# Performance work log

Hardware: AMD Instinct MI355X
Metric: run time of the kernel (lower is better)

Reference implementation:

```python
import jax, jax.numpy as jnp
import numpy as np

DIM, HEADS, WIN = 256, 8, 8
HD = DIM // HEADS
SCALE = HD ** -0.5


def _rel_index(w):
    # Swin-style relative position index, computed statically in numpy
    coords = np.stack(np.meshgrid(np.arange(w), np.arange(w), indexing='ij'))  # (2,w,w)
    cf = coords.reshape(2, -1)                      # (2, w*w)
    rel = (cf[:, :, None] - cf[:, None, :]).transpose(1, 2, 0)  # (w*w, w*w, 2)
    rel = rel.copy()
    rel[:, :, 0] += w - 1
    rel[:, :, 1] += w - 1
    rel[:, :, 0] *= 2 * w - 1
    return rel.sum(-1)                              # (w*w, w*w)

REL_IDX = _rel_index(WIN)


def setup_inputs() -> dict:
    key = jax.random.key(0)
    ks = jax.random.split(key, 6)
    B, C, D, H, W = 8, DIM, 100, WIN, WIN
    return {
        'x': jax.random.normal(ks[0], (B, C, D, H, W), jnp.float32),
        'dwconv_w': jax.random.normal(ks[1], (C, C, 1, 3, 3), jnp.float32) * 0.02,
        'dwconv_b': jnp.zeros((C,), jnp.float32),
        'qkv_w': jax.random.normal(ks[2], (3 * C, C), jnp.float32) * 0.02,
        'qkv_b': jnp.zeros((3 * C,), jnp.float32),
        'proj_w': jax.random.normal(ks[3], (C, C), jnp.float32) * 0.02,
        'proj_b': jnp.zeros((C,), jnp.float32),
        'rpb_table': jax.random.normal(ks[4], ((2 * WIN - 1) ** 2, HEADS), jnp.float32) * 0.02,
    }


def reference(x, dwconv_w, dwconv_b, qkv_w, qkv_b, proj_w, proj_b, rpb_table):
    B, C, D, H, W = x.shape
    N = H * W
    # 'dwconv': full Conv3d, kernel (1,3,3), padding (0,1,1)
    xl = jax.lax.conv_general_dilated(
        x, dwconv_w, window_strides=(1, 1, 1),
        padding=[(0, 0), (1, 1), (1, 1)],
        dimension_numbers=('NCDHW', 'OIDHW', 'NCDHW'),
    ) + dwconv_b[None, :, None, None, None]
    # qkv: 1x1x1 conv == pointwise linear over channels
    qkv = jnp.einsum('oc,bcdhw->bodhw', qkv_w, xl) + qkv_b[None, :, None, None, None]
    # channel dim layout: (three, head, head_dim)
    qkv = qkv.reshape(B, 3, HEADS, HD, D, N)
    q, k, v = qkv[:, 0], qkv[:, 1], qkv[:, 2]      # each (B, HEADS, HD, D, N)
    attn = jnp.einsum('bhcdn,bhcdm->bdhnm', q * SCALE, k)  # (B, D, HEADS, N, N)
    bias = rpb_table[REL_IDX.reshape(-1)].reshape(N, N, HEADS).transpose(2, 0, 1)
    attn = jax.nn.softmax(attn + bias[None, None], axis=-1)
    xa = jnp.einsum('bdhnm,bhcdm->bhcdn', attn, v)  # (B, HEADS, HD, D, N)
    xa = xa.reshape(B, C, D, H, W)                  # channel = (head, head_dim)
    out = jnp.einsum('oc,bcdhw->bodhw', proj_w, xa) + proj_b[None, :, None, None, None]
    return out
```

## Files before the change

kernel.cpp:

```cpp
#include <hip/hip_runtime.h>
#include <cstdint>
#include <cstddef>

#define SCALEQ 0.17677669529663689f

typedef _Float16 half_t;
typedef _Float16 half8   __attribute__((ext_vector_type(8)));
typedef _Float16 half4v  __attribute__((ext_vector_type(4)));
typedef float    float4v __attribute__((ext_vector_type(4)));

#define GLDS16(gp, lp)                                                        \
  __builtin_amdgcn_global_load_lds(                                           \
      (const __attribute__((address_space(1))) void*)(gp),                    \
      (__attribute__((address_space(3))) void*)(lp), 16, 0, 0)

__global__ __launch_bounds__(256) void prep_all(
    const float* __restrict__ x, const float* __restrict__ dwconv_w,
    const float* __restrict__ qkv_w, const float* __restrict__ proj_w,
    const float* __restrict__ rpb, half_t* __restrict__ xpad,
    half_t* __restrict__ Wt, half_t* __restrict__ qw16,
    half_t* __restrict__ pw16, float* __restrict__ btab) {
  __shared__ float tile[128 * 65];
  const int blk = blockIdx.x, t = threadIdx.x;
  if (blk < 800) {
    const int bd = blk, b = bd / 100, d = bd % 100;
    for (int hf = 0; hf < 2; ++hf) {
      for (int i = 0; i < 32; ++i) {
        int idx = i * 256 + t, c = idx >> 6, hw = idx & 63;
        tile[c * 65 + hw] = x[(size_t)((b * 256 + hf * 128 + c) * 100 + d) * 64 + hw];
      }
      __syncthreads();
      for (int i = 0; i < 50; ++i) {
        int idx = i * 256 + t, cell = idx >> 7, c = idx & 127;
        int hh = cell / 10, ww = cell % 10;
        float v = 0.f;
        if (hh >= 1 && hh <= 8 && ww >= 1 && ww <= 8)
          v = tile[c * 65 + (hh - 1) * 8 + (ww - 1)];
        xpad[(size_t)(bd * 100 + cell) * 256 + hf * 128 + c] = (half_t)v;
      }
      __syncthreads();
    }
  } else if (blk < 944) {
    const int base = (blk - 800) * 4096;
#pragma unroll
    for (int i = 0; i < 16; ++i) {
      int idx = base + i * 256 + t;
      int tap = idx >> 16;
      int og = (idx >> 12) & 15, kh = (idx >> 9) & 7;
      int l15o = (idx >> 5) & 15, c5 = idx & 31;
      int o = og * 16 + l15o, c = kh * 32 + c5;
      Wt[idx] = (half_t)dwconv_w[(o * 256 + c) * 9 + tap];
    }
  } else if (blk < 1040) {
    const int base = (blk - 944) * 2048;
#pragma unroll
    for (int i = 0; i < 8; ++i) {
      int idx = base + i * 256 + t;
      float v = qkv_w[idx];
      if (idx < 65536) v *= SCALEQ;
      qw16[idx] = (half_t)v;
    }
  } else if (blk < 1072) {
    const int base = (blk - 1040) * 2048;
#pragma unroll
    for (int i = 0; i < 8; ++i) {
      int idx = base + i * 256 + t;
      pw16[idx] = (half_t)proj_w[idx];
    }
  } else {
    const int base = (blk - 1072) * 2048;
#pragma unroll
    for (int i = 0; i < 8; ++i) {
      int idx = base + i * 256 + t;
      int hd = idx >> 12, n = (idx >> 6) & 63, m = idx & 63;
      int h1 = n >> 3, w1 = n & 7, h2 = m >> 3, w2 = m & 7;
      int ridx = (h1 - h2 + 7) * 15 + (w1 - w2 + 7);
      btab[idx] = rpb[ridx * 8 + hd];
    }
  }
}

__global__ __launch_bounds__(512) void fused_all(
    const half_t* __restrict__ xpg, const half_t* __restrict__ Wt,
    const float* __restrict__ convb, const half_t* __restrict__ qw,
    const float* __restrict__ qkvb, const float* __restrict__ btab,
    const half_t* __restrict__ pw, const float* __restrict__ projb,
    float* __restrict__ out32) {
  __shared__ __align__(16) half_t LS[78336];
  const int bd = blockIdx.x;
  const int tid = threadIdx.x;
  const int wave = tid >> 6, lane = tid & 63;
  const int l15 = lane & 15, quad = lane >> 4;
  const int head = wave;

  half_t* xlp = LS;
  half_t* xa = LS;
  float* T = (float*)LS;
  half_t* xpl = LS + 16896;
  half_t* scr = LS + 16896 + wave * 7680;
  half_t* qsc = scr;
  half_t* ksc = scr + 2560;
  half_t* vsc = scr + 5120;
  half_t* Psc = scr;

  const half_t* Wq0 = qw + head * 32 * 256;
  const half_t* Wk0 = qw + 65536 + head * 32 * 256;
  const half_t* Wv0 = qw + 131072 + head * 32 * 256;

  {
    const char* src = (const char*)(xpg + (size_t)bd * 25600);
    const int cid = wave * 64 + lane;
#pragma unroll
    for (int i = 0; i < 7; ++i) {
      const int chunkid = i * 512 + cid;
      if (chunkid < 3200) {
        const int cell = chunkid >> 5, p = chunkid & 31;
        const int g = (p & 24) | ((p ^ cell) & 7);
        GLDS16(src + cell * 512 + g * 16,
               (char*)xpl + (i * 512 + wave * 64) * 16);
      }
    }
  }
  __syncthreads();

  {
    const int pxb = (l15 >> 3) * 10 + (l15 & 7);
    float4v acc[2][4];
#pragma unroll
    for (int mi = 0; mi < 2; ++mi)
#pragma unroll
      for (int ni = 0; ni < 4; ++ni) {
        float4v z = {0.f, 0.f, 0.f, 0.f};
        acc[mi][ni] = z;
      }
    const half_t* wv0 = Wt + (wave * 2) * 4096 + l15 * 32 + quad * 8;
#pragma unroll 1
    for (int tap = 0; tap < 9; ++tap) {
      const int tc = (tap / 3) * 10 + (tap % 3);
      const half_t* wt = wv0 + tap * 65536;
      const int c0 = pxb + tc;
#pragma unroll
      for (int kh = 0; kh < 8; ++kh) {
        half8 af0 = *(const half8*)(wt + kh * 512);
        half8 af1 = *(const half8*)(wt + 4096 + kh * 512);
        half8 bf[4];
#pragma unroll
        for (int ni = 0; ni < 4; ++ni) {
          const int cell = c0 + ni * 20;
          bf[ni] = *(const half8*)&xpl[cell * 256 + (((kh * 4 + quad) ^ (cell & 7)) * 8)];
        }
#pragma unroll
        for (int ni = 0; ni < 4; ++ni) {
          acc[0][ni] = __builtin_amdgcn_mfma_f32_16x16x32_f16(af0, bf[ni], acc[0][ni], 0, 0, 0);
          acc[1][ni] = __builtin_amdgcn_mfma_f32_16x16x32_f16(af1, bf[ni], acc[1][ni], 0, 0, 0);
        }
      }
    }
#pragma unroll
    for (int mi = 0; mi < 2; ++mi) {
      const int o4 = wave * 32 + mi * 16 + quad * 4;
      const float4v b4 = *(const float4v*)&convb[o4];
      const int chunk = o4 >> 3;
      const int sub = (quad & 1) * 4;
#pragma unroll
      for (int ni = 0; ni < 4; ++ni) {
        const int px = ni * 16 + l15;
        half4v h;
        h.x = (half_t)(acc[mi][ni].x + b4.x);
        h.y = (half_t)(acc[mi][ni].y + b4.y);
        h.z = (half_t)(acc[mi][ni].z + b4.z);
        h.w = (half_t)(acc[mi][ni].w + b4.w);
        *(half4v*)&xlp[px * 256 + ((chunk ^ (px & 7)) * 8) + sub] = h;
      }
    }
  }

  half8 wq[8][2];
#pragma unroll
  for (int kh = 0; kh < 8; ++kh)
#pragma unroll
    for (int mi = 0; mi < 2; ++mi)
      wq[kh][mi] = *(const half8*)(Wq0 + (mi * 16 + l15) * 256 + kh * 32 + quad * 8);

  __syncthreads();

  half8 wk[8][2];
  {
    float4v acc[2][4];
#pragma unroll
    for (int mi = 0; mi < 2; ++mi)
#pragma unroll
      for (int ni = 0; ni < 4; ++ni) {
        float4v z = {0.f, 0.f, 0.f, 0.f};
        acc[mi][ni] = z;
      }
#pragma unroll
    for (int kh = 0; kh < 8; ++kh) {
      half8 bf[4];
#pragma unroll
      for (int ni = 0; ni < 4; ++ni) {
        int r = ni * 16 + l15;
        bf[ni] = *(const half8*)&xlp[r * 256 + (((kh * 4 + quad) ^ (r & 7)) * 8)];
      }
#pragma unroll
      for (int mi = 0; mi < 2; ++mi)
        wk[kh][mi] = *(const half8*)(Wk0 + (mi * 16 + l15) * 256 + kh * 32 + quad * 8);
#pragma unroll
      for (int mi = 0; mi < 2; ++mi)
#pragma unroll
        for (int ni = 0; ni < 4; ++ni)
          acc[mi][ni] = __builtin_amdgcn_mfma_f32_16x16x32_f16(
              wq[kh][mi], bf[ni], acc[mi][ni], 0, 0, 0);
    }
#pragma unroll
    for (int mi = 0; mi < 2; ++mi) {
      const float4v b4 = *(const float4v*)&qkvb[head * 32 + mi * 16 + quad * 4];
#pragma unroll
      for (int ni = 0; ni < 4; ++ni) {
        half4v h;
        h.x = (half_t)(acc[mi][ni].x + b4.x * SCALEQ);
        h.y = (half_t)(acc[mi][ni].y + b4.y * SCALEQ);
        h.z = (half_t)(acc[mi][ni].z + b4.z * SCALEQ);
        h.w = (half_t)(acc[mi][ni].w + b4.w * SCALEQ);
        *(half4v*)(qsc + (ni * 16 + l15) * 40 + mi * 16 + quad * 4) = h;
      }
    }
  }

  half8 wv[8][2];
  {
    float4v acc[2][4];
#pragma unroll
    for (int mi = 0; mi < 2; ++mi)
#pragma unroll
      for (int ni = 0; ni < 4; ++ni) {
        float4v z = {0.f, 0.f, 0.f, 0.f};
        acc[mi][ni] = z;
      }
#pragma unroll
    for (int kh = 0; kh < 8; ++kh) {
      half8 bf[4];
#pragma unroll
      for (int ni = 0; ni < 4; ++ni) {
        int r = ni * 16 + l15;
        bf[ni] = *(const half8*)&xlp[r * 256 + (((kh * 4 + quad) ^ (r & 7)) * 8)];
      }
#pragma unroll
      for (int mi = 0; mi < 2; ++mi)
        wv[kh][mi] = *(const half8*)(Wv0 + (mi * 16 + l15) * 256 + kh * 32 + quad * 8);
#pragma unroll
      for (int mi = 0; mi < 2; ++mi)
#pragma unroll
        for (int ni = 0; ni < 4; ++ni)
          acc[mi][ni] = __builtin_amdgcn_mfma_f32_16x16x32_f16(
              wk[kh][mi], bf[ni], acc[mi][ni], 0, 0, 0);
    }
#pragma unroll
    for (int mi = 0; mi < 2; ++mi) {
      const float4v b4 = *(const float4v*)&qkvb[256 + head * 32 + mi * 16 + quad * 4];
#pragma unroll
      for (int ni = 0; ni < 4; ++ni) {
        half4v h;
        h.x = (half_t)(acc[mi][ni].x + b4.x);
        h.y = (half_t)(acc[mi][ni].y + b4.y);
        h.z = (half_t)(acc[mi][ni].z + b4.z);
        h.w = (half_t)(acc[mi][ni].w + b4.w);
        *(half4v*)(ksc + (ni * 16 + l15) * 40 + mi * 16 + quad * 4) = h;
      }
    }
  }

  {
    float4v acc[2][4];
#pragma unroll
    for (int mi = 0; mi < 2; ++mi)
#pragma unroll
      for (int ni = 0; ni < 4; ++ni) {
        float4v z = {0.f, 0.f, 0.f, 0.f};
        acc[mi][ni] = z;
      }
#pragma unroll
    for (int kh = 0; kh < 8; ++kh) {
      half8 bf[4];
#pragma unroll
      for (int ni = 0; ni < 4; ++ni) {
        int r = ni * 16 + l15;
        bf[ni] = *(const half8*)&xlp[r * 256 + (((kh * 4 + quad) ^ (r & 7)) * 8)];
      }
#pragma unroll
      for (int mi = 0; mi < 2; ++mi)
#pragma unroll
        for (int ni = 0; ni < 4; ++ni)
          acc[mi][ni] = __builtin_amdgcn_mfma_f32_16x16x32_f16(
              wv[kh][mi], bf[ni], acc[mi][ni], 0, 0, 0);
    }
#pragma unroll
    for (int mi = 0; mi < 2; ++mi) {
      const float4v b4 = *(const float4v*)&qkvb[512 + head * 32 + mi * 16 + quad * 4];
#pragma unroll
      for (int ni = 0; ni < 4; ++ni) {
#pragma unroll
        for (int iv = 0; iv < 4; ++iv)
          vsc[(mi * 16 + quad * 4 + iv) * 72 + ni * 16 + l15] =
              (half_t)(acc[mi][ni][iv] + b4[iv]);
      }
    }
  }

  __builtin_amdgcn_s_waitcnt(0);

  half8 aq[4], bk[4];
#pragma unroll
  for (int i = 0; i < 4; ++i) {
    aq[i] = *(const half8*)(qsc + (i * 16 + l15) * 40 + quad * 8);
    bk[i] = *(const half8*)(ksc + (i * 16 + l15) * 40 + quad * 8);
  }
  const float* bh = btab + head * 4096;
  float br[4][4][4];
#pragma unroll
  for (int ni = 0; ni < 4; ++ni)
#pragma unroll
    for (int i = 0; i < 4; ++i) {
      const int n = ni * 16 + quad * 4 + i;
#pragma unroll
      for (int mi = 0; mi < 4; ++mi)
        br[ni][i][mi] = bh[n * 64 + mi * 16 + l15];
    }
  float4v s[4][4];
#pragma unroll
  for (int ni = 0; ni < 4; ++ni)
#pragma unroll
    for (int mi = 0; mi < 4; ++mi) {
      float4v z = {0.f, 0.f, 0.f, 0.f};
      s[ni][mi] = __builtin_amdgcn_mfma_f32_16x16x32_f16(aq[ni], bk[mi], z, 0, 0, 0);
    }
#pragma unroll
  for (int ni = 0; ni < 4; ++ni)
#pragma unroll
    for (int i = 0; i < 4; ++i)
#pragma unroll
      for (int mi = 0; mi < 4; ++mi) s[ni][mi][i] += br[ni][i][mi];
  float inv[4][4];
#pragma unroll
  for (int ni = 0; ni < 4; ++ni)
#pragma unroll
    for (int i = 0; i < 4; ++i) {
      float mx = fmaxf(fmaxf(s[ni][0][i], s[ni][1][i]), fmaxf(s[ni][2][i], s[ni][3][i]));
      for (int off = 1; off < 16; off <<= 1) mx = fmaxf(mx, __shfl_xor(mx, off));
      float sum = 0.f;
#pragma unroll
      for (int mi = 0; mi < 4; ++mi) {
        float e = __expf(s[ni][mi][i] - mx);
        s[ni][mi][i] = e;
        sum += e;
      }
      for (int off = 1; off < 16; off <<= 1) sum += __shfl_xor(sum, off);
      inv[ni][i] = 1.0f / sum;
    }
#pragma unroll
  for (int ni = 0; ni < 4; ++ni)
#pragma unroll
    for (int i = 0; i < 4; ++i) {
      const int n = ni * 16 + quad * 4 + i;
#pragma unroll
      for (int mi = 0; mi < 4; ++mi)
        Psc[n * 72 + mi * 16 + l15] = (half_t)(s[ni][mi][i] * inv[ni][i]);
    }
  __builtin_amdgcn_s_waitcnt(0);

  half8 wp[8][2];
#pragma unroll
  for (int kh = 0; kh < 8; ++kh)
#pragma unroll
    for (int mi = 0; mi < 2; ++mi)
      wp[kh][mi] = *(const half8*)(pw + (wave * 32 + mi * 16 + l15) * 256 + kh * 32 + quad * 8);
  half8 av[2][2];
#pragma unroll
  for (int ci = 0; ci < 2; ++ci)
#pragma unroll
    for (int k2 = 0; k2 < 2; ++k2)
      av[ci][k2] = *(const half8*)(vsc + (ci * 16 + l15) * 72 + k2 * 32 + quad * 8);
  float4v oa[2][4];
#pragma unroll
  for (int ci = 0; ci < 2; ++ci)
#pragma unroll
    for (int ni = 0; ni < 4; ++ni) {
      float4v z = {0.f, 0.f, 0.f, 0.f};
      oa[ci][ni] = z;
    }
#pragma unroll
  for (int ni = 0; ni < 4; ++ni)
#pragma unroll
    for (int k2 = 0; k2 < 2; ++k2) {
      half8 bp = *(const half8*)&Psc[(ni * 16 + l15) * 72 + k2 * 32 + quad * 8];
#pragma unroll
      for (int ci = 0; ci < 2; ++ci)
        oa[ci][ni] = __builtin_amdgcn_mfma_f32_16x16x32_f16(av[ci][k2], bp, oa[ci][ni], 0, 0, 0);
    }

  __syncthreads();

#pragma unroll
  for (int ci = 0; ci < 2; ++ci)
#pragma unroll
    for (int ni = 0; ni < 4; ++ni) {
      half4v h = {(half_t)oa[ci][ni].x, (half_t)oa[ci][ni].y,
                  (half_t)oa[ci][ni].z, (half_t)oa[ci][ni].w};
      *(half4v*)(xa + (ni * 16 + l15) * 264 + head * 32 + ci * 16 + quad * 4) = h;
    }
  __syncthreads();

  float4v pacc[2][4];
#pragma unroll
  for (int mi = 0; mi < 2; ++mi)
#pragma unroll
    for (int ni = 0; ni < 4; ++ni) {
      float4v z = {0.f, 0.f, 0.f, 0.f};
      pacc[mi][ni] = z;
    }
#pragma unroll
  for (int kh = 0; kh < 8; ++kh) {
    half8 bf[4];
#pragma unroll
    for (int ni = 0; ni < 4; ++ni)
      bf[ni] = *(const half8*)&xa[(ni * 16 + l15) * 264 + kh * 32 + quad * 8];
#pragma unroll
    for (int mi = 0; mi < 2; ++mi)
#pragma unroll
      for (int ni = 0; ni < 4; ++ni)
        pacc[mi][ni] = __builtin_amdgcn_mfma_f32_16x16x32_f16(
            wp[kh][mi], bf[ni], pacc[mi][ni], 0, 0, 0);
  }
#pragma unroll
  for (int mi = 0; mi < 2; ++mi) {
    const float4v b4 = *(const float4v*)&projb[wave * 32 + mi * 16 + quad * 4];
#pragma unroll
    for (int ni = 0; ni < 4; ++ni) {
      pacc[mi][ni].x += b4.x;
      pacc[mi][ni].y += b4.y;
      pacc[mi][ni].z += b4.z;
      pacc[mi][ni].w += b4.w;
    }
  }

  const int b = bd / 100, d = bd % 100;
  const size_t bdbase = (size_t)b * 1638400 + (size_t)d * 64;
  const int tr = tid >> 3;
  const int col0 = (tid & 7) * 8;
  for (int r = 0; r < 4; ++r) {
    __syncthreads();
    if ((wave >> 1) == r) {
      const int rb = (wave & 1) * 32;
#pragma unroll
      for (int mi = 0; mi < 2; ++mi)
#pragma unroll
        for (int ni = 0; ni < 4; ++ni)
#pragma unroll
          for (int iv = 0; iv < 4; ++iv)
            T[(rb + mi * 16 + quad * 4 + iv) * 68 + ni * 16 + l15] = pacc[mi][ni][iv];
    }
    __syncthreads();
    const int o = r * 64 + tr;
    float* dst = out32 + bdbase + (size_t)o * 6400 + col0;
    const float* srcT = &T[tr * 68 + col0];
    *(float4v*)dst = *(const float4v*)srcT;
    *(float4v*)(dst + 4) = *(const float4v*)(srcT + 4);
  }
}

extern "C" void kernel_launch(void* const* d_in, const int* in_sizes, int n_in,
                              void* d_out, int out_size, void* d_ws, size_t ws_size,
                              hipStream_t stream) {
  const float* x        = (const float*)d_in[0];
  const float* dwconv_w = (const float*)d_in[1];
  const float* dwconv_b = (const float*)d_in[2];
  const float* qkv_w    = (const float*)d_in[3];
  const float* qkv_b    = (const float*)d_in[4];
  const float* proj_w   = (const float*)d_in[5];
  const float* proj_b   = (const float*)d_in[6];
  const float* rpb      = (const float*)d_in[7];
  float* out = (float*)d_out;

  char* ws = (char*)d_ws;
  size_t off = 0;
  half_t* xpad = (half_t*)(ws + off); off += 40960000;
  half_t* Wt   = (half_t*)(ws + off); off += 1179648;
  half_t* qw16 = (half_t*)(ws + off); off += 393216;
  half_t* pw16 = (half_t*)(ws + off); off += 131072;
  float*  btab = (float*)(ws + off);  off += 131072;

  prep_all<<<1088, 256, 0, stream>>>(x, dwconv_w, qkv_w, proj_w, rpb,
                                     xpad, Wt, qw16, pw16, btab);
  fused_all<<<800, 512, 0, stream>>>(xpad, Wt, dwconv_b, qw16, qkv_b, btab,
                                     pw16, proj_b, out);
}
```

Before: 310.2 us.

## Drop padded input buffer, shrink LDS per wave and reuse one scratch buffer

The intermediate fp16 input no longer stores a 10x10 zero-padded grid. It stores only the 64 real pixels plus a single shared zero row in LDS, and the conv taps redirect out-of-range pixels to that row. This cuts global write and read traffic for the intermediate. Per-wave scratch is collapsed into one reused 2560-element buffer, with Q/K/V and the softmax probabilities staged through it in pieces. Total LDS drops from ~153KB to ~72KB, and launch bounds request more resident blocks to raise occupancy. The cost is extra LDS round trips and waits in the attention phase, and it depends on the compiler fitting the register budget that those launch bounds imply.

```diff
diff --git a/kernel.cpp b/kernel.cpp
--- a/kernel.cpp
+++ b/kernel.cpp
@@ -14,10 +14,16 @@
       (const __attribute__((address_space(1))) void*)(gp),                    \
       (__attribute__((address_space(3))) void*)(lp), 16, 0, 0)
 
+#define WAIT_LDS()                                                            \
+  do {                                                                        \
+    asm volatile("s_waitcnt lgkmcnt(0)" ::: "memory");                        \
+    __builtin_amdgcn_sched_barrier(0);                                        \
+  } while (0)
+
 __global__ __launch_bounds__(256) void prep_all(
     const float* __restrict__ x, const float* __restrict__ dwconv_w,
     const float* __restrict__ qkv_w, const float* __restrict__ proj_w,
-    const float* __restrict__ rpb, half_t* __restrict__ xpad,
+    const float* __restrict__ rpb, half_t* __restrict__ xq,
     half_t* __restrict__ Wt, half_t* __restrict__ qw16,
     half_t* __restrict__ pw16, float* __restrict__ btab) {
   __shared__ float tile[128 * 65];
@@ -30,13 +36,14 @@
         tile[c * 65 + hw] = x[(size_t)((b * 256 + hf * 128 + c) * 100 + d) * 64 + hw];
       }
       __syncthreads();
-      for (int i = 0; i < 50; ++i) {
-        int idx = i * 256 + t, cell = idx >> 7, c = idx & 127;
-        int hh = cell / 10, ww = cell % 10;
-        float v = 0.f;
-        if (hh >= 1 && hh <= 8 && ww >= 1 && ww <= 8)
-          v = tile[c * 65 + (hh - 1) * 8 + (ww - 1)];
-        xpad[(size_t)(bd * 100 + cell) * 256 + hf * 128 + c] = (half_t)v;
+#pragma unroll
+      for (int i = 0; i < 4; ++i) {
+        int chunk = i * 256 + t;
+        int hw = chunk >> 4, c8 = chunk & 15;
+        half8 h;
+#pragma unroll
+        for (int j = 0; j < 8; ++j) h[j] = (half_t)tile[(c8 * 8 + j) * 65 + hw];
+        *(half8*)(xq + (size_t)(bd * 64 + hw) * 256 + hf * 128 + c8 * 8) = h;
       }
       __syncthreads();
     }
@@ -80,13 +87,13 @@
   }
 }
 
-__global__ __launch_bounds__(512) void fused_all(
-    const half_t* __restrict__ xpg, const half_t* __restrict__ Wt,
+__global__ __launch_bounds__(512, 4) void fused_all(
+    const half_t* __restrict__ xqg, const half_t* __restrict__ Wt,
     const float* __restrict__ convb, const half_t* __restrict__ qw,
     const float* __restrict__ qkvb, const float* __restrict__ btab,
     const half_t* __restrict__ pw, const float* __restrict__ projb,
     float* __restrict__ out32) {
-  __shared__ __align__(16) half_t LS[78336];
+  __shared__ __align__(16) half_t LS[36864];
   const int bd = blockIdx.x;
   const int tid = threadIdx.x;
   const int wave = tid >> 6, lane = tid & 63;
@@ -96,35 +103,32 @@
   half_t* xlp = LS;
   half_t* xa = LS;
   float* T = (float*)LS;
-  half_t* xpl = LS + 16896;
-  half_t* scr = LS + 16896 + wave * 7680;
-  half_t* qsc = scr;
-  half_t* ksc = scr + 2560;
-  half_t* vsc = scr + 5120;
-  half_t* Psc = scr;
+  half_t* xpl = LS + 16384;
+  half_t* buf = LS + 16384 + wave * 2560;
 
   const half_t* Wq0 = qw + head * 32 * 256;
   const half_t* Wk0 = qw + 65536 + head * 32 * 256;
   const half_t* Wv0 = qw + 131072 + head * 32 * 256;
 
   {
-    const char* src = (const char*)(xpg + (size_t)bd * 25600);
+    const char* src = (const char*)(xqg + (size_t)bd * 16384);
     const int cid = wave * 64 + lane;
 #pragma unroll
-    for (int i = 0; i < 7; ++i) {
+    for (int i = 0; i < 4; ++i) {
       const int chunkid = i * 512 + cid;
-      if (chunkid < 3200) {
-        const int cell = chunkid >> 5, p = chunkid & 31;
-        const int g = (p & 24) | ((p ^ cell) & 7);
-        GLDS16(src + cell * 512 + g * 16,
-               (char*)xpl + (i * 512 + wave * 64) * 16);
-      }
+      const int row = chunkid >> 5, p = chunkid & 31;
+      const int g = (p & 24) | ((p ^ row) & 7);
+      GLDS16(src + row * 512 + g * 16, (char*)xpl + (i * 512 + wave * 64) * 16);
+    }
+    if (tid < 32) {
+      half8 z = {};
+      *(half8*)(xpl + 64 * 256 + tid * 8) = z;
     }
   }
   __syncthreads();
 
   {
-    const int pxb = (l15 >> 3) * 10 + (l15 & 7);
+    const int wwl = l15 & 7, hb = l15 >> 3;
     float4v acc[2][4];
 #pragma unroll
     for (int mi = 0; mi < 2; ++mi)
@@ -136,9 +140,17 @@
     const half_t* wv0 = Wt + (wave * 2) * 4096 + l15 * 32 + quad * 8;
 #pragma unroll 1
     for (int tap = 0; tap < 9; ++tap) {
-      const int tc = (tap / 3) * 10 + (tap % 3);
+      const int th = tap / 3, tw = tap - th * 3;
       const half_t* wt = wv0 + tap * 65536;
-      const int c0 = pxb + tc;
+      const int ww = wwl + tw;
+      const int okw = (ww >= 1) & (ww <= 8);
+      int rowv[4];
+#pragma unroll
+      for (int ni = 0; ni < 4; ++ni) {
+        const int hh = hb + th + ni * 2;
+        const int ok = okw & (hh >= 1) & (hh <= 8);
+        rowv[ni] = ok ? ((hh - 1) * 8 + (ww - 1)) : 64;
+      }
 #pragma unroll
       for (int kh = 0; kh < 8; ++kh) {
         half8 af0 = *(const half8*)(wt + kh * 512);
@@ -146,8 +158,8 @@
         half8 bf[4];
 #pragma unroll
         for (int ni = 0; ni < 4; ++ni) {
-          const int cell = c0 + ni * 20;
-          bf[ni] = *(const half8*)&xpl[cell * 256 + (((kh * 4 + quad) ^ (cell & 7)) * 8)];
+          const int r = rowv[ni];
+          bf[ni] = *(const half8*)&xpl[r * 256 + (((kh * 4 + quad) ^ (r & 7)) * 8)];
         }
 #pragma unroll
         for (int ni = 0; ni < 4; ++ni) {
@@ -184,6 +196,7 @@
 
   __syncthreads();
 
+  half8 aq[4];
   half8 wk[8][2];
   {
     float4v acc[2][4];
@@ -222,11 +235,17 @@
         h.y = (half_t)(acc[mi][ni].y + b4.y * SCALEQ);
         h.z = (half_t)(acc[mi][ni].z + b4.z * SCALEQ);
         h.w = (half_t)(acc[mi][ni].w + b4.w * SCALEQ);
-        *(half4v*)(qsc + (ni * 16 + l15) * 40 + mi * 16 + quad * 4) = h;
-      }
-    }
-  }
-
+        *(half4v*)(buf + (ni * 16 + l15) * 40 + mi * 16 + quad * 4) = h;
+      }
+    }
+    WAIT_LDS();
+#pragma unroll
+    for (int i = 0; i < 4; ++i)
+      aq[i] = *(const half8*)(buf + (i * 16 + l15) * 40 + quad * 8);
+    WAIT_LDS();
+  }
+
+  half8 bk[4];
   half8 wv[8][2];
   {
     float4v acc[2][4];
@@ -265,9 +284,14 @@
         h.y = (half_t)(acc[mi][ni].y + b4.y);
         h.z = (half_t)(acc[mi][ni].z + b4.z);
         h.w = (half_t)(acc[mi][ni].w + b4.w);
-        *(half4v*)(ksc + (ni * 16 + l15) * 40 + mi * 16 + quad * 4) = h;
-      }
-    }
+        *(half4v*)(buf + (ni * 16 + l15) * 40 + mi * 16 + quad * 4) = h;
+      }
+    }
+    WAIT_LDS();
+#pragma unroll
+    for (int i = 0; i < 4; ++i)
+      bk[i] = *(const half8*)(buf + (i * 16 + l15) * 40 + quad * 8);
+    WAIT_LDS();
   }
 
   {
@@ -301,20 +325,12 @@
       for (int ni = 0; ni < 4; ++ni) {
 #pragma unroll
         for (int iv = 0; iv < 4; ++iv)
-          vsc[(mi * 16 + quad * 4 + iv) * 72 + ni * 16 + l15] =
+          buf[(mi * 16 + quad * 4 + iv) * 72 + ni * 16 + l15] =
               (half_t)(acc[mi][ni][iv] + b4[iv]);
       }
     }
   }
 
-  __builtin_amdgcn_s_waitcnt(0);
-
-  half8 aq[4], bk[4];
-#pragma unroll
-  for (int i = 0; i < 4; ++i) {
-    aq[i] = *(const half8*)(qsc + (i * 16 + l15) * 40 + quad * 8);
-    bk[i] = *(const half8*)(ksc + (i * 16 + l15) * 40 + quad * 8);
-  }
   const float* bh = btab + head * 4096;
   float br[4][4][4];
 #pragma unroll
@@ -357,29 +373,16 @@
       for (int off = 1; off < 16; off <<= 1) sum += __shfl_xor(sum, off);
       inv[ni][i] = 1.0f / sum;
     }
-#pragma unroll
-  for (int ni = 0; ni < 4; ++ni)
-#pragma unroll
-    for (int i = 0; i < 4; ++i) {
-      const int n = ni * 16 + quad * 4 + i;
-#pragma unroll
-      for (int mi = 0; mi < 4; ++mi)
-        Psc[n * 72 + mi * 16 + l15] = (half_t)(s[ni][mi][i] * inv[ni][i]);
-    }
-  __builtin_amdgcn_s_waitcnt(0);
-
-  half8 wp[8][2];
-#pragma unroll
-  for (int kh = 0; kh < 8; ++kh)
-#pragma unroll
-    for (int mi = 0; mi < 2; ++mi)
-      wp[kh][mi] = *(const half8*)(pw + (wave * 32 + mi * 16 + l15) * 256 + kh * 32 + quad * 8);
+
+  WAIT_LDS();
   half8 av[2][2];
 #pragma unroll
   for (int ci = 0; ci < 2; ++ci)
 #pragma unroll
     for (int k2 = 0; k2 < 2; ++k2)
-      av[ci][k2] = *(const half8*)(vsc + (ci * 16 + l15) * 72 + k2 * 32 + quad * 8);
+      av[ci][k2] = *(const half8*)(buf + (ci * 16 + l15) * 72 + k2 * 32 + quad * 8);
+  WAIT_LDS();
+
   float4v oa[2][4];
 #pragma unroll
   for (int ci = 0; ci < 2; ++ci)
@@ -389,14 +392,37 @@
       oa[ci][ni] = z;
     }
 #pragma unroll
-  for (int ni = 0; ni < 4; ++ni)
-#pragma unroll
-    for (int k2 = 0; k2 < 2; ++k2) {
-      half8 bp = *(const half8*)&Psc[(ni * 16 + l15) * 72 + k2 * 32 + quad * 8];
+  for (int k2 = 0; k2 < 2; ++k2) {
+#pragma unroll
+    for (int mi2 = 0; mi2 < 2; ++mi2) {
+      const int mi = k2 * 2 + mi2;
+#pragma unroll
+      for (int ni = 0; ni < 4; ++ni)
+#pragma unroll
+        for (int i = 0; i < 4; ++i) {
+          const int n = ni * 16 + quad * 4 + i;
+          buf[n * 40 + mi2 * 16 + l15] = (half_t)(s[ni][mi][i] * inv[ni][i]);
+        }
+    }
+    WAIT_LDS();
+    half8 bp[4];
+#pragma unroll
+    for (int ni = 0; ni < 4; ++ni)
+      bp[ni] = *(const half8*)(buf + (ni * 16 + l15) * 40 + quad * 8);
+    WAIT_LDS();
+#pragma unroll
+    for (int ni = 0; ni < 4; ++ni)
 #pragma unroll
       for (int ci = 0; ci < 2; ++ci)
-        oa[ci][ni] = __builtin_amdgcn_mfma_f32_16x16x32_f16(av[ci][k2], bp, oa[ci][ni], 0, 0, 0);
-    }
+        oa[ci][ni] = __builtin_amdgcn_mfma_f32_16x16x32_f16(av[ci][k2], bp[ni], oa[ci][ni], 0, 0, 0);
+  }
+
+  half8 wp[8][2];
+#pragma unroll
+  for (int kh = 0; kh < 8; ++kh)
+#pragma unroll
+    for (int mi = 0; mi < 2; ++mi)
+      wp[kh][mi] = *(const half8*)(pw + (wave * 32 + mi * 16 + l15) * 256 + kh * 32 + quad * 8);
 
   __syncthreads();
 
@@ -483,14 +509,14 @@
 
   char* ws = (char*)d_ws;
   size_t off = 0;
-  half_t* xpad = (half_t*)(ws + off); off += 40960000;
+  half_t* xq   = (half_t*)(ws + off); off += 26214400;
   half_t* Wt   = (half_t*)(ws + off); off += 1179648;
   half_t* qw16 = (half_t*)(ws + off); off += 393216;
   half_t* pw16 = (half_t*)(ws + off); off += 131072;
   float*  btab = (float*)(ws + off);  off += 131072;
 
   prep_all<<<1088, 256, 0, stream>>>(x, dwconv_w, qkv_w, proj_w, rpb,
-                                     xpad, Wt, qw16, pw16, btab);
-  fused_all<<<800, 512, 0, stream>>>(xpad, Wt, dwconv_b, qw16, qkv_b, btab,
+                                     xq, Wt, qw16, pw16, btab);
+  fused_all<<<800, 512, 0, stream>>>(xq, Wt, dwconv_b, qw16, qkv_b, btab,
                                      pw16, proj_b, out);
 }
```

Result: faster. 295.1 us (-4.9%).

## Split conv into its own kernel reading fp32 input directly, drop padded staging buffer

Applied to the files above, without the earlier changes.

Removes the separate padded fp16 transpose pass and folds the x transpose and fp16 conversion into a new conv kernel. Zero padding is handled with a shared zero row and index clamping instead of a materialised 10x10 halo. The conv output goes through a global fp16 buffer that a slimmed attention/proj kernel reads back. This trades the xpad write and read for an extra xl round trip and an extra launch, while lowering LDS use and possibly raising occupancy in each kernel.

```diff
diff --git a/kernel.cpp b/kernel.cpp
--- a/kernel.cpp
+++ b/kernel.cpp
@@ -14,34 +14,14 @@
       (const __attribute__((address_space(1))) void*)(gp),                    \
       (__attribute__((address_space(3))) void*)(lp), 16, 0, 0)
 
-__global__ __launch_bounds__(256) void prep_all(
-    const float* __restrict__ x, const float* __restrict__ dwconv_w,
-    const float* __restrict__ qkv_w, const float* __restrict__ proj_w,
-    const float* __restrict__ rpb, half_t* __restrict__ xpad,
+__global__ __launch_bounds__(256) void prep_w(
+    const float* __restrict__ dwconv_w, const float* __restrict__ qkv_w,
+    const float* __restrict__ proj_w, const float* __restrict__ rpb,
     half_t* __restrict__ Wt, half_t* __restrict__ qw16,
     half_t* __restrict__ pw16, float* __restrict__ btab) {
-  __shared__ float tile[128 * 65];
   const int blk = blockIdx.x, t = threadIdx.x;
-  if (blk < 800) {
-    const int bd = blk, b = bd / 100, d = bd % 100;
-    for (int hf = 0; hf < 2; ++hf) {
-      for (int i = 0; i < 32; ++i) {
-        int idx = i * 256 + t, c = idx >> 6, hw = idx & 63;
-        tile[c * 65 + hw] = x[(size_t)((b * 256 + hf * 128 + c) * 100 + d) * 64 + hw];
-      }
-      __syncthreads();
-      for (int i = 0; i < 50; ++i) {
-        int idx = i * 256 + t, cell = idx >> 7, c = idx & 127;
-        int hh = cell / 10, ww = cell % 10;
-        float v = 0.f;
-        if (hh >= 1 && hh <= 8 && ww >= 1 && ww <= 8)
-          v = tile[c * 65 + (hh - 1) * 8 + (ww - 1)];
-        xpad[(size_t)(bd * 100 + cell) * 256 + hf * 128 + c] = (half_t)v;
-      }
-      __syncthreads();
-    }
-  } else if (blk < 944) {
-    const int base = (blk - 800) * 4096;
+  if (blk < 144) {
+    const int base = blk * 4096;
 #pragma unroll
     for (int i = 0; i < 16; ++i) {
       int idx = base + i * 256 + t;
@@ -51,8 +31,8 @@
       int o = og * 16 + l15o, c = kh * 32 + c5;
       Wt[idx] = (half_t)dwconv_w[(o * 256 + c) * 9 + tap];
     }
-  } else if (blk < 1040) {
-    const int base = (blk - 944) * 2048;
+  } else if (blk < 240) {
+    const int base = (blk - 144) * 2048;
 #pragma unroll
     for (int i = 0; i < 8; ++i) {
       int idx = base + i * 256 + t;
@@ -60,15 +40,15 @@
       if (idx < 65536) v *= SCALEQ;
       qw16[idx] = (half_t)v;
     }
-  } else if (blk < 1072) {
-    const int base = (blk - 1040) * 2048;
+  } else if (blk < 272) {
+    const int base = (blk - 240) * 2048;
 #pragma unroll
     for (int i = 0; i < 8; ++i) {
       int idx = base + i * 256 + t;
       pw16[idx] = (half_t)proj_w[idx];
     }
   } else {
-    const int base = (blk - 1072) * 2048;
+    const int base = (blk - 272) * 2048;
 #pragma unroll
     for (int i = 0; i < 8; ++i) {
       int idx = base + i * 256 + t;
@@ -80,9 +60,113 @@
   }
 }
 
-__global__ __launch_bounds__(512) void fused_all(
-    const half_t* __restrict__ xpg, const half_t* __restrict__ Wt,
-    const float* __restrict__ convb, const half_t* __restrict__ qw,
+__global__ __launch_bounds__(512) void conv_std(
+    const float* __restrict__ xg, const half_t* __restrict__ Wt,
+    const float* __restrict__ convb, half_t* __restrict__ xl) {
+  __shared__ __align__(16) half_t LS[16640];
+  const int bd = blockIdx.x;
+  const int tid = threadIdx.x;
+  const int wave = tid >> 6, lane = tid & 63;
+  const int l15 = lane & 15, quad = lane >> 4;
+  const int b = bd / 100, d = bd % 100;
+
+  half_t* xpl = LS;
+  float* tile = (float*)LS;
+
+  half8 xr[4];
+  {
+    const float* xb0 = xg + ((size_t)(b * 256) * 100 + d) * 64;
+    for (int hf = 0; hf < 2; ++hf) {
+#pragma unroll
+      for (int i = 0; i < 16; ++i) {
+        const int cl = i * 8 + wave;
+        tile[cl * 65 + lane] = xb0[(size_t)(hf * 128 + cl) * 6400 + lane];
+      }
+      __syncthreads();
+#pragma unroll
+      for (int ii = 0; ii < 2; ++ii) {
+        const int c8l = wave * 2 + ii;
+#pragma unroll
+        for (int j = 0; j < 8; ++j)
+          xr[hf * 2 + ii][j] = (half_t)tile[(c8l * 8 + j) * 65 + lane];
+      }
+      __syncthreads();
+    }
+#pragma unroll
+    for (int hf = 0; hf < 2; ++hf)
+#pragma unroll
+      for (int ii = 0; ii < 2; ++ii) {
+        const int c8 = hf * 16 + wave * 2 + ii;
+        *(half8*)&xpl[lane * 256 + ((c8 ^ (lane & 7)) * 8)] = xr[hf * 2 + ii];
+      }
+    if (tid < 32) {
+      half8 z = {};
+      *(half8*)(xpl + 64 * 256 + tid * 8) = z;
+    }
+  }
+  __syncthreads();
+
+  {
+    const int wwl = l15 & 7, hb = l15 >> 3;
+    float4v acc[2][4];
+#pragma unroll
+    for (int mi = 0; mi < 2; ++mi)
+#pragma unroll
+      for (int ni = 0; ni < 4; ++ni) {
+        float4v z = {0.f, 0.f, 0.f, 0.f};
+        acc[mi][ni] = z;
+      }
+    const half_t* wv0 = Wt + (wave * 2) * 4096 + l15 * 32 + quad * 8;
+#pragma unroll 1
+    for (int tap = 0; tap < 9; ++tap) {
+      const int th = tap / 3, tw = tap - th * 3;
+      const half_t* wt = wv0 + tap * 65536;
+      const int ww = wwl + tw;
+      const int okw = (ww >= 1) & (ww <= 8);
+      int rowv[4];
+#pragma unroll
+      for (int ni = 0; ni < 4; ++ni) {
+        const int hh = hb + th + ni * 2;
+        const int ok = okw & (hh >= 1) & (hh <= 8);
+        rowv[ni] = ok ? ((hh - 1) * 8 + (ww - 1)) : 64;
+      }
+#pragma unroll
+      for (int kh = 0; kh < 8; ++kh) {
+        half8 af0 = *(const half8*)(wt + kh * 512);
+        half8 af1 = *(const half8*)(wt + 4096 + kh * 512);
+        half8 bf[4];
+#pragma unroll
+        for (int ni = 0; ni < 4; ++ni) {
+          const int r = rowv[ni];
+          bf[ni] = *(const half8*)&xpl[r * 256 + (((kh * 4 + quad) ^ (r & 7)) * 8)];
+        }
+#pragma unroll
+        for (int ni = 0; ni < 4; ++ni) {
+          acc[0][ni] = __builtin_amdgcn_mfma_f32_16x16x32_f16(af0, bf[ni], acc[0][ni], 0, 0, 0);
+          acc[1][ni] = __builtin_amdgcn_mfma_f32_16x16x32_f16(af1, bf[ni], acc[1][ni], 0, 0, 0);
+        }
+      }
+    }
+#pragma unroll
+    for (int mi = 0; mi < 2; ++mi) {
+      const int o4 = wave * 32 + mi * 16 + quad * 4;
+      const float4v b4 = *(const float4v*)&convb[o4];
+#pragma unroll
+      for (int ni = 0; ni < 4; ++ni) {
+        const int px = ni * 16 + l15;
+        half4v h;
+        h.x = (half_t)(acc[mi][ni].x + b4.x);
+        h.y = (half_t)(acc[mi][ni].y + b4.y);
+        h.z = (half_t)(acc[mi][ni].z + b4.z);
+        h.w = (half_t)(acc[mi][ni].w + b4.w);
+        *(half4v*)(xl + (size_t)bd * 16384 + px * 256 + o4) = h;
+      }
+    }
+  }
+}
+
+__global__ __launch_bounds__(512) void fused_tail4(
+    const half_t* __restrict__ xlg, const half_t* __restrict__ qw,
     const float* __restrict__ qkvb, const float* __restrict__ btab,
     const half_t* __restrict__ pw, const float* __restrict__ projb,
     float* __restrict__ out32) {
@@ -96,7 +180,6 @@
   half_t* xlp = LS;
   half_t* xa = LS;
   float* T = (float*)LS;
-  half_t* xpl = LS + 16896;
   half_t* scr = LS + 16896 + wave * 7680;
   half_t* qsc = scr;
   half_t* ksc = scr + 2560;
@@ -107,81 +190,22 @@
   const half_t* Wk0 = qw + 65536 + head * 32 * 256;
   const half_t* Wv0 = qw + 131072 + head * 32 * 256;
 
+  half8 wq[8][2];
+#pragma unroll
+  for (int kh = 0; kh < 8; ++kh)
+#pragma unroll
+    for (int mi = 0; mi < 2; ++mi)
+      wq[kh][mi] = *(const half8*)(Wq0 + (mi * 16 + l15) * 256 + kh * 32 + quad * 8);
+
   {
-    const char* src = (const char*)(xpg + (size_t)bd * 25600);
-    const int cid = wave * 64 + lane;
-#pragma unroll
-    for (int i = 0; i < 7; ++i) {
-      const int chunkid = i * 512 + cid;
-      if (chunkid < 3200) {
-        const int cell = chunkid >> 5, p = chunkid & 31;
-        const int g = (p & 24) | ((p ^ cell) & 7);
-        GLDS16(src + cell * 512 + g * 16,
-               (char*)xpl + (i * 512 + wave * 64) * 16);
-      }
-    }
-  }
-  __syncthreads();
-
-  {
-    const int pxb = (l15 >> 3) * 10 + (l15 & 7);
-    float4v acc[2][4];
-#pragma unroll
-    for (int mi = 0; mi < 2; ++mi)
-#pragma unroll
-      for (int ni = 0; ni < 4; ++ni) {
-        float4v z = {0.f, 0.f, 0.f, 0.f};
-        acc[mi][ni] = z;
-      }
-    const half_t* wv0 = Wt + (wave * 2) * 4096 + l15 * 32 + quad * 8;
-#pragma unroll 1
-    for (int tap = 0; tap < 9; ++tap) {
-      const int tc = (tap / 3) * 10 + (tap % 3);
-      const half_t* wt = wv0 + tap * 65536;
-      const int c0 = pxb + tc;
-#pragma unroll
-      for (int kh = 0; kh < 8; ++kh) {
-        half8 af0 = *(const half8*)(wt + kh * 512);
-        half8 af1 = *(const half8*)(wt + 4096 + kh * 512);
-        half8 bf[4];
-#pragma unroll
-        for (int ni = 0; ni < 4; ++ni) {
-          const int cell = c0 + ni * 20;
-          bf[ni] = *(const half8*)&xpl[cell * 256 + (((kh * 4 + quad) ^ (cell & 7)) * 8)];
-        }
-#pragma unroll
-        for (int ni = 0; ni < 4; ++ni) {
-          acc[0][ni] = __builtin_amdgcn_mfma_f32_16x16x32_f16(af0, bf[ni], acc[0][ni], 0, 0, 0);
-          acc[1][ni] = __builtin_amdgcn_mfma_f32_16x16x32_f16(af1, bf[ni], acc[1][ni], 0, 0, 0);
-        }
-      }
-    }
-#pragma unroll
-    for (int mi = 0; mi < 2; ++mi) {
-      const int o4 = wave * 32 + mi * 16 + quad * 4;
-      const float4v b4 = *(const float4v*)&convb[o4];
-      const int chunk = o4 >> 3;
-      const int sub = (quad & 1) * 4;
-#pragma unroll
-      for (int ni = 0; ni < 4; ++ni) {
-        const int px = ni * 16 + l15;
-        half4v h;
-        h.x = (half_t)(acc[mi][ni].x + b4.x);
-        h.y = (half_t)(acc[mi][ni].y + b4.y);
-        h.z = (half_t)(acc[mi][ni].z + b4.z);
-        h.w = (half_t)(acc[mi][ni].w + b4.w);
-        *(half4v*)&xlp[px * 256 + ((chunk ^ (px & 7)) * 8) + sub] = h;
-      }
-    }
-  }
-
-  half8 wq[8][2];
-#pragma unroll
-  for (int kh = 0; kh < 8; ++kh)
-#pragma unroll
-    for (int mi = 0; mi < 2; ++mi)
-      wq[kh][mi] = *(const half8*)(Wq0 + (mi * 16 + l15) * 256 + kh * 32 + quad * 8);
-
+    const char* src = (const char*)(xlg + (size_t)bd * 64 * 256);
+#pragma unroll
+    for (int i = 0; i < 4; ++i) {
+      int row = i * 16 + wave * 2 + (lane >> 5);
+      int sch = (lane & 31) ^ (row & 7);
+      GLDS16(src + row * 512 + sch * 16, (char*)xlp + (i * 16 + wave * 2) * 512);
+    }
+  }
   __syncthreads();
 
   half8 wk[8][2];
@@ -483,14 +507,14 @@
 
   char* ws = (char*)d_ws;
   size_t off = 0;
-  half_t* xpad = (half_t*)(ws + off); off += 40960000;
+  half_t* xl   = (half_t*)(ws + off); off += 26214400;
   half_t* Wt   = (half_t*)(ws + off); off += 1179648;
   half_t* qw16 = (half_t*)(ws + off); off += 393216;
   half_t* pw16 = (half_t*)(ws + off); off += 131072;
   float*  btab = (float*)(ws + off);  off += 131072;
 
-  prep_all<<<1088, 256, 0, stream>>>(x, dwconv_w, qkv_w, proj_w, rpb,
-                                     xpad, Wt, qw16, pw16, btab);
-  fused_all<<<800, 512, 0, stream>>>(xpad, Wt, dwconv_b, qw16, qkv_b, btab,
-                                     pw16, proj_b, out);
+  prep_w<<<288, 256, 0, stream>>>(dwconv_w, qkv_w, proj_w, rpb,
+                                  Wt, qw16, pw16, btab);
+  conv_std<<<800, 512, 0, stream>>>(x, Wt, dwconv_b, xl);
+  fused_tail4<<<800, 512, 0, stream>>>(xl, qw16, qkv_b, btab, pw16, proj_b, out);
 }
```

After: 270.6 us. 12.8% less time.
